# Kernel tuning notes

Measured on AMD Instinct MI355X. Metric: run time of the kernel, lower is better.

Reference implementation:

```python
import jax, jax.numpy as jnp
import numpy as np

B, N, M, C, S = 4, 16384, 128, 128, 512  # batch, points, boxes, feat dim, sampled pts


def setup_inputs() -> dict:
    key = jax.random.key(0)
    k1, k2, k3, k4, k5, k6, k7 = jax.random.split(key, 7)
    # point cloud roughly in a LiDAR extent
    xy = jax.random.uniform(k1, (B, N, 2), minval=-50.0, maxval=50.0)
    z = jax.random.uniform(k2, (B, N, 1), minval=-3.0, maxval=3.0)
    points = jnp.concatenate([xy, z], axis=-1).astype(jnp.float32)
    point_features = jax.random.normal(k3, (B, N, C), dtype=jnp.float32)
    # boxes: (cx, cy, cz_bottom, dx, dy, dz, rz)
    ctr_xy = jax.random.uniform(k4, (B, M, 2), minval=-50.0, maxval=50.0)
    ctr_z = jax.random.uniform(k5, (B, M, 1), minval=-3.0, maxval=0.0)
    sizes = jax.random.uniform(k6, (B, M, 3), minval=2.0, maxval=8.0)
    rz = jax.random.uniform(k7, (B, M, 1), minval=-np.pi, maxval=np.pi)
    boxes3d = jnp.concatenate([ctr_xy, ctr_z, sizes, rz], axis=-1).astype(jnp.float32)
    return {"points": points, "point_features": point_features, "boxes3d": boxes3d}


def _pool_one_box(points, feats, box):
    # points (N,3), feats (N,C), box (7,)
    n = points.shape[0]
    cx, cy, cz, dx, dy, dz, rz = box
    cz = cz + 0.5 * dz  # bottom center -> geometric center (mmcv convention)
    sx = points[:, 0] - cx
    sy = points[:, 1] - cy
    cosa = jnp.cos(-rz)
    sina = jnp.sin(-rz)
    lx = sx * cosa - sy * sina
    ly = sx * sina + sy * cosa
    mask = (
        (jnp.abs(points[:, 2] - cz) <= 0.5 * dz)
        & (lx > -0.5 * dx) & (lx < 0.5 * dx)
        & (ly > -0.5 * dy) & (ly < 0.5 * dy)
    )
    cnt = mask.sum(dtype=jnp.int32)
    # rank of each in-box point among in-box points (first-come order)
    rank = jnp.cumsum(mask.astype(jnp.int32)) - 1
    pos = jnp.where(mask, rank, n)  # out-of-range for non-members -> dropped
    table = jnp.zeros((n,), jnp.int32).at[pos].set(
        jnp.arange(n, dtype=jnp.int32), mode="drop")
    # wrap-around duplication when cnt < S (kernel copies k % cnt)
    j = jnp.arange(S, dtype=jnp.int32) % jnp.maximum(cnt, 1)
    idx = table[j]  # (S,)
    pooled = jnp.concatenate([points[idx], feats[idx]], axis=-1)  # (S, 3+C)
    pooled = jnp.where(cnt > 0, pooled, jnp.zeros_like(pooled))
    empty = (cnt == 0).astype(jnp.int32)
    return pooled, empty


def reference(points, point_features, boxes3d):
    # vmap over boxes, then over batch
    per_scene = jax.vmap(_pool_one_box, in_axes=(None, None, 0))
    per_batch = jax.vmap(per_scene, in_axes=(0, 0, 0))
    pooled_features, pooled_empty_flag = per_batch(points, point_features, boxes3d)
    return pooled_features, pooled_empty_flag
```

## Files before the change

kernel.cpp:

```cpp
#include <hip/hip_runtime.h>

#define B_ 4
#define N_ 16384
#define M_ 128
#define C_ 128
#define S_ 512
#define ROW_ (3 + C_)
#define NCHUNK_ 256
#define TILE_ 128
#define RSTR_ 132

typedef float f4_t __attribute__((ext_vector_type(4)));

__global__ __launch_bounds__(256) void mask_kernel(
    const float* __restrict__ points,
    const float* __restrict__ boxes,
    unsigned long long* __restrict__ masks,
    int* __restrict__ cnts)
{
    const int gwave = blockIdx.x * 4 + (threadIdx.x >> 6);
    const int lane  = threadIdx.x & 63;
    const int bm    = gwave >> 4;
    const int seg   = gwave & 15;
    const int b     = bm >> 7;

    const float* bx = boxes + bm * 7;
    const float cx = bx[0], cy = bx[1], czb = bx[2];
    const float dx = bx[3], dy = bx[4], dzv = bx[5], rz = bx[6];
    const float cz   = __fadd_rn(czb, __fmul_rn(0.5f, dzv));
    const float cosa = (float)cos(-(double)rz);
    const float sina = (float)sin(-(double)rz);
    const float hdx = 0.5f * dx, hdy = 0.5f * dy, hdz = 0.5f * dzv;

    const float* pb = points + (size_t)b * N_ * 3;

    #pragma unroll 4
    for (int k = 0; k < 16; ++k) {
        const int chunk = seg * 16 + k;
        const int i = chunk * 64 + lane;
        const float x = pb[i*3+0], y = pb[i*3+1], z = pb[i*3+2];
        const float sx = __fsub_rn(x, cx);
        const float sy = __fsub_rn(y, cy);
        const float lx = __fsub_rn(__fmul_rn(sx, cosa), __fmul_rn(sy, sina));
        const float ly = __fadd_rn(__fmul_rn(sx, sina), __fmul_rn(sy, cosa));
        const bool pred = (fabsf(__fsub_rn(z, cz)) <= hdz) &&
                          (lx > -hdx) && (lx < hdx) &&
                          (ly > -hdy) && (ly < hdy);
        const unsigned long long m = __ballot(pred);
        if (lane == 0) {
            masks[(size_t)bm * NCHUNK_ + chunk] = m;
            cnts [(size_t)bm * NCHUNK_ + chunk] = __popcll(m);
        }
    }
}

__global__ __launch_bounds__(256) void pool_kernel(
    const float* __restrict__ points,
    const float* __restrict__ feats,
    const unsigned long long* __restrict__ masks,
    const int* __restrict__ cnts,
    float* __restrict__ out,
    float* __restrict__ flags_out)
{
    const int bm  = blockIdx.x;
    const int b   = bm >> 7;
    const int tid = threadIdx.x;

    __shared__ int   sc[NCHUNK_];
    __shared__ int   s_idx[S_];
    __shared__ int   jtab[S_];
    __shared__ float srow[TILE_ * RSTR_];

    const int c = cnts[(size_t)bm * NCHUNK_ + tid];
    sc[tid] = c;
    __syncthreads();
    for (int off = 1; off < NCHUNK_; off <<= 1) {
        const int v = (tid >= off) ? sc[tid - off] : 0;
        __syncthreads();
        sc[tid] += v;
        __syncthreads();
    }
    const int total = sc[NCHUNK_ - 1];
    const int P = sc[tid] - c;

    if (c > 0 && P < S_) {
        unsigned long long m = masks[(size_t)bm * NCHUNK_ + tid];
        int pos = P;
        while (m && pos < S_) {
            const int bit = __ffsll((unsigned long long)m) - 1;
            m &= m - 1;
            s_idx[pos++] = tid * 64 + bit;
        }
    }
    __syncthreads();

    const int cnt_eff = total < S_ ? total : S_;
    const int denom   = cnt_eff > 0 ? cnt_eff : 1;

    for (int s = tid; s < S_; s += 256) jtab[s] = s % denom;

    const int T = cnt_eff < TILE_ ? cnt_eff : TILE_;
    if (total == 0) {
        for (int e = tid; e < RSTR_; e += 256) srow[e] = 0.0f;
    } else {
        const int nf4 = T * 32;
        for (int t = tid; t < nf4; t += 256) {
            const int u = t >> 5, q = t & 31;
            const size_t pbase = (size_t)b * N_ + (unsigned)s_idx[u];
            const f4_t v = *(const f4_t*)(feats + pbase * C_ + q * 4);
            *(f4_t*)(srow + u * RSTR_ + q * 4) = v;
        }
        for (int t = tid; t < T * 3; t += 256) {
            const int u = t / 3, k = t - u * 3;
            const size_t pbase = (size_t)b * N_ + (unsigned)s_idx[u];
            srow[u * RSTR_ + 128 + k] = points[pbase * 3 + k];
        }
    }
    __syncthreads();

    float* ob = out + (size_t)bm * (S_ * ROW_);
    for (int f = tid; f < (S_ * ROW_) / 4; f += 256) {
        const int e = f * 4;
        f4_t v;
        #pragma unroll
        for (int jj = 0; jj < 4; ++jj) {
            const unsigned ee = (unsigned)(e + jj);
            const unsigned s  = ee / (unsigned)ROW_;
            const int col = (int)(ee - s * ROW_);
            const int j = jtab[s];
            float val;
            if (j < TILE_) {
                val = (col < 3) ? srow[j * RSTR_ + 128 + col]
                                : srow[j * RSTR_ + (col - 3)];
            } else {
                const size_t pbase = (size_t)b * N_ + (unsigned)s_idx[j];
                val = (col < 3) ? points[pbase * 3 + col]
                                : feats[pbase * C_ + (col - 3)];
            }
            v[jj] = val;
        }
        __builtin_nontemporal_store(v, (f4_t*)(ob + e));
    }
    if (tid == 0) flags_out[bm] = (total == 0) ? 1.0f : 0.0f;
}

extern "C" void kernel_launch(void* const* d_in, const int* in_sizes, int n_in,
                              void* d_out, int out_size, void* d_ws, size_t ws_size,
                              hipStream_t stream) {
    const float* points = (const float*)d_in[0];
    const float* feats  = (const float*)d_in[1];
    const float* boxes  = (const float*)d_in[2];
    float* out = (float*)d_out;

    unsigned long long* masks = (unsigned long long*)d_ws;
    int* cnts = (int*)((char*)d_ws + (size_t)B_ * M_ * NCHUNK_ * 8);

    float* flags = out + (size_t)B_ * M_ * S_ * ROW_;

    mask_kernel<<<B_ * M_ * 16 / 4, 256, 0, stream>>>(points, boxes, masks, cnts);
    pool_kernel<<<B_ * M_, 256, 0, stream>>>(points, feats, masks, cnts, out, flags);
}
```

Before: 201.2 us.

## Reuse loaded points across boxes and swizzle pooled-row shared memory layout

The mask kernel now loads each wave's 1024 points into registers once and tests them against four boxes, which cuts redundant point loads and quarters the grid. The pool kernel stores cached rows in shared memory with a swizzled layout (row stride 136, columns interleaved by col mod 4) so that output assembly reads with fewer bank conflicts. The output loop also computes the row division once per float4 and takes a fast path when both rows touched are cached. The costs are higher register pressure in the mask kernel, fewer blocks in flight, and scalar rather than vector shared-memory stores.

Result: faster. 187.2 us (-6.9%).

```diff
diff --git a/kernel.cpp b/kernel.cpp
--- a/kernel.cpp
+++ b/kernel.cpp
@@ -5,12 +5,17 @@
 #define M_ 128
 #define C_ 128
 #define S_ 512
-#define ROW_ (3 + C_)
+#define ROW_ 131
 #define NCHUNK_ 256
 #define TILE_ 128
-#define RSTR_ 132
+#define LSTR_ 136
+#define KBOX_ 4
 
 typedef float f4_t __attribute__((ext_vector_type(4)));
+
+__device__ __forceinline__ int swz(int j, int col) {
+    return j * LSTR_ + (col & 3) * 34 + (col >> 2);
+}
 
 __global__ __launch_bounds__(256) void mask_kernel(
     const float* __restrict__ points,
@@ -20,36 +25,44 @@
 {
     const int gwave = blockIdx.x * 4 + (threadIdx.x >> 6);
     const int lane  = threadIdx.x & 63;
-    const int bm    = gwave >> 4;
+    const int grp   = gwave >> 4;
     const int seg   = gwave & 15;
-    const int b     = bm >> 7;
-
-    const float* bx = boxes + bm * 7;
-    const float cx = bx[0], cy = bx[1], czb = bx[2];
-    const float dx = bx[3], dy = bx[4], dzv = bx[5], rz = bx[6];
-    const float cz   = __fadd_rn(czb, __fmul_rn(0.5f, dzv));
-    const float cosa = (float)cos(-(double)rz);
-    const float sina = (float)sin(-(double)rz);
-    const float hdx = 0.5f * dx, hdy = 0.5f * dy, hdz = 0.5f * dzv;
+    const int bm0   = grp * KBOX_;
+    const int b     = bm0 >> 7;
 
     const float* pb = points + (size_t)b * N_ * 3;
+    float px[16], py[16], pz[16];
+    #pragma unroll
+    for (int k = 0; k < 16; ++k) {
+        const int i = (seg * 16 + k) * 64 + lane;
+        px[k] = pb[i*3+0]; py[k] = pb[i*3+1]; pz[k] = pb[i*3+2];
+    }
 
-    #pragma unroll 4
-    for (int k = 0; k < 16; ++k) {
-        const int chunk = seg * 16 + k;
-        const int i = chunk * 64 + lane;
-        const float x = pb[i*3+0], y = pb[i*3+1], z = pb[i*3+2];
-        const float sx = __fsub_rn(x, cx);
-        const float sy = __fsub_rn(y, cy);
-        const float lx = __fsub_rn(__fmul_rn(sx, cosa), __fmul_rn(sy, sina));
-        const float ly = __fadd_rn(__fmul_rn(sx, sina), __fmul_rn(sy, cosa));
-        const bool pred = (fabsf(__fsub_rn(z, cz)) <= hdz) &&
-                          (lx > -hdx) && (lx < hdx) &&
-                          (ly > -hdy) && (ly < hdy);
-        const unsigned long long m = __ballot(pred);
-        if (lane == 0) {
-            masks[(size_t)bm * NCHUNK_ + chunk] = m;
-            cnts [(size_t)bm * NCHUNK_ + chunk] = __popcll(m);
+    for (int kb = 0; kb < KBOX_; ++kb) {
+        const int bm = bm0 + kb;
+        const float* bx = boxes + bm * 7;
+        const float cx = bx[0], cy = bx[1], czb = bx[2];
+        const float dx = bx[3], dy = bx[4], dzv = bx[5], rz = bx[6];
+        const float cz   = __fadd_rn(czb, __fmul_rn(0.5f, dzv));
+        const float cosa = (float)cos(-(double)rz);
+        const float sina = (float)sin(-(double)rz);
+        const float hdx = 0.5f * dx, hdy = 0.5f * dy, hdz = 0.5f * dzv;
+
+        #pragma unroll
+        for (int k = 0; k < 16; ++k) {
+            const float sx = __fsub_rn(px[k], cx);
+            const float sy = __fsub_rn(py[k], cy);
+            const float lx = __fsub_rn(__fmul_rn(sx, cosa), __fmul_rn(sy, sina));
+            const float ly = __fadd_rn(__fmul_rn(sx, sina), __fmul_rn(sy, cosa));
+            const bool pred = (fabsf(__fsub_rn(pz[k], cz)) <= hdz) &&
+                              (lx > -hdx) && (lx < hdx) &&
+                              (ly > -hdy) && (ly < hdy);
+            const unsigned long long m = __ballot(pred);
+            if (lane == 0) {
+                const int chunk = seg * 16 + k;
+                masks[(size_t)bm * NCHUNK_ + chunk] = m;
+                cnts [(size_t)bm * NCHUNK_ + chunk] = __popcll(m);
+            }
         }
     }
 }
@@ -68,8 +81,8 @@
 
     __shared__ int   sc[NCHUNK_];
     __shared__ int   s_idx[S_];
-    __shared__ int   jtab[S_];
-    __shared__ float srow[TILE_ * RSTR_];
+    __shared__ int   jtab[S_ + 1];
+    __shared__ float srow[TILE_ * LSTR_];
 
     const int c = cnts[(size_t)bm * NCHUNK_ + tid];
     sc[tid] = c;
@@ -96,48 +109,62 @@
 
     const int cnt_eff = total < S_ ? total : S_;
     const int denom   = cnt_eff > 0 ? cnt_eff : 1;
-
-    for (int s = tid; s < S_; s += 256) jtab[s] = s % denom;
+    for (int s = tid; s <= S_; s += 256) jtab[s] = (s < S_) ? (s % denom) : 0;
 
     const int T = cnt_eff < TILE_ ? cnt_eff : TILE_;
     if (total == 0) {
-        for (int e = tid; e < RSTR_; e += 256) srow[e] = 0.0f;
+        if (tid < LSTR_) srow[tid] = 0.0f;
     } else {
         const int nf4 = T * 32;
         for (int t = tid; t < nf4; t += 256) {
             const int u = t >> 5, q = t & 31;
             const size_t pbase = (size_t)b * N_ + (unsigned)s_idx[u];
             const f4_t v = *(const f4_t*)(feats + pbase * C_ + q * 4);
-            *(f4_t*)(srow + u * RSTR_ + q * 4) = v;
+            #pragma unroll
+            for (int jj = 0; jj < 4; ++jj)
+                srow[swz(u, 3 + 4 * q + jj)] = v[jj];
         }
         for (int t = tid; t < T * 3; t += 256) {
             const int u = t / 3, k = t - u * 3;
             const size_t pbase = (size_t)b * N_ + (unsigned)s_idx[u];
-            srow[u * RSTR_ + 128 + k] = points[pbase * 3 + k];
+            srow[swz(u, k)] = points[pbase * 3 + k];
         }
     }
     __syncthreads();
 
     float* ob = out + (size_t)bm * (S_ * ROW_);
     for (int f = tid; f < (S_ * ROW_) / 4; f += 256) {
-        const int e = f * 4;
+        const int e = 4 * f;
+        const unsigned s0 = (unsigned)e / (unsigned)ROW_;
+        const int col0 = e - (int)s0 * ROW_;
+        const int ja = jtab[s0], jb = jtab[s0 + 1];
         f4_t v;
-        #pragma unroll
-        for (int jj = 0; jj < 4; ++jj) {
-            const unsigned ee = (unsigned)(e + jj);
-            const unsigned s  = ee / (unsigned)ROW_;
-            const int col = (int)(ee - s * ROW_);
-            const int j = jtab[s];
-            float val;
-            if (j < TILE_) {
-                val = (col < 3) ? srow[j * RSTR_ + 128 + col]
-                                : srow[j * RSTR_ + (col - 3)];
-            } else {
-                const size_t pbase = (size_t)b * N_ + (unsigned)s_idx[j];
-                val = (col < 3) ? points[pbase * 3 + col]
-                                : feats[pbase * C_ + (col - 3)];
+        if ((ja < TILE_) & (jb < TILE_)) {
+            #pragma unroll
+            for (int jj = 0; jj < 4; ++jj) {
+                int col = col0 + jj;
+                const bool cross = col >= ROW_;
+                col = cross ? col - ROW_ : col;
+                const int j = cross ? jb : ja;
+                v[jj] = srow[swz(j, col)];
             }
-            v[jj] = val;
+        } else {
+            #pragma unroll
+            for (int jj = 0; jj < 4; ++jj) {
+                int col = col0 + jj;
+                unsigned s = s0;
+                if (col >= ROW_) { col -= ROW_; ++s; }
+                const int j = jtab[s];
+                float val;
+                if (j < TILE_) {
+                    val = srow[swz(j, col)];
+                } else {
+                    const size_t pbase = (size_t)b * N_ + (unsigned)s_idx[j];
+                    val = (col < 3) ? points[pbase * 3 + col]
+                                    : feats[pbase * C_ + (col - 3)];
+                }
+                v[jj] = val;
+            }
         }
         __builtin_nontemporal_store(v, (f4_t*)(ob + e));
     }
@@ -157,6 +184,7 @@
 
     float* flags = out + (size_t)B_ * M_ * S_ * ROW_;
 
-    mask_kernel<<<B_ * M_ * 16 / 4, 256, 0, stream>>>(points, boxes, masks, cnts);
+    mask_kernel<<<B_ * M_ * 16 / 4 / KBOX_, 256, 0, stream>>>(
+        points, boxes, masks, cnts);
     pool_kernel<<<B_ * M_, 256, 0, stream>>>(points, feats, masks, cnts, out, flags);
 }
```
